# Kernel tuning notes

Measured on AMD Instinct MI355X. Metric: run time of the kernel, lower is better.

Reference implementation:

```python
import jax, jax.numpy as jnp
import numpy as np

B, T, M = 8, 512, 80
U = 896          # RNN_Size (even)
C = 256          # Class


def setup_inputs() -> dict:
    key = jax.random.key(0)
    ks = jax.random.split(key, 13)
    s = 0.05
    d = {
        'mels': jax.random.normal(ks[0], (B, T, M), jnp.float32),
        'Wk':  jax.random.normal(ks[1], (M + 3, 3 * U), jnp.float32) * s,
        'Wr':  jax.random.normal(ks[2], (U, 3 * U), jnp.float32) * s,
        'b':   jax.random.normal(ks[3], (2, 3 * U), jnp.float32) * s,
        'W1c': jax.random.normal(ks[4], (U // 2, U // 2), jnp.float32) * s,
        'b1c': jax.random.normal(ks[5], (U // 2,), jnp.float32) * s,
        'W2c': jax.random.normal(ks[6], (U // 2, C), jnp.float32) * s,
        'b2c': jax.random.normal(ks[7], (C,), jnp.float32) * s,
        'W1f': jax.random.normal(ks[8], (U // 2, U // 2), jnp.float32) * s,
        'b1f': jax.random.normal(ks[9], (U // 2,), jnp.float32) * s,
        'W2f': jax.random.normal(ks[10], (U // 2, C), jnp.float32) * s,
        'b2f': jax.random.normal(ks[11], (C,), jnp.float32) * s,
    }
    return d


def reference(mels, Wk, Wr, b, W1c, b1c, W2c, b2c, W1f, b1f, W2f, b2f):
    # Keras GRUCell (reset_after=True) step.
    def gru(x, h):
        mx = x @ Wk + b[0]                     # [B, 3U]
        mi = h @ Wr + b[1]                     # [B, 3U]
        xz, xr, xh = jnp.split(mx, 3, axis=-1)
        iz, ir, ih = jnp.split(mi, 3, axis=-1)
        z = jax.nn.sigmoid(xz + iz)
        r = jax.nn.sigmoid(xr + ir)
        hh = jnp.tanh(xh + r * ih)
        return z * h + (1.0 - z) * hh

    def head(h, W1, b1, W2, b2):
        return jax.nn.relu(h @ W1 + b1) @ W2 + b2

    Bv = mels.shape[0]
    Tv = mels.shape[1]
    keys = jax.random.split(jax.random.key(42), Tv)
    mels_t = jnp.swapaxes(mels, 0, 1)          # [T, B, M]

    def step(carry, xs):
        coarse, fine, hidden = carry           # [B,1],[B,1],[B,U]
        mel, key = xs
        kc, kf = jax.random.split(key)
        dummy = jnp.zeros_like(coarse)
        # coarse pass (hidden NOT updated, faithful to original)
        x0 = jnp.concatenate([mel, coarse, fine, dummy], axis=-1)
        h0 = gru(x0, hidden)
        logit_c = head(h0[:, :U // 2], W1c, b1c, W2c, b2c)
        # original feeds softmax probs into tf.random.categorical (which
        # expects logits) -- reproduce that faithfully.
        probs_c = jax.nn.softmax(logit_c, axis=-1)
        new_c = jax.random.categorical(kc, probs_c, axis=-1).astype(mels.dtype)[:, None]
        new_c_val = new_c / 255.0 * 2.0 - 1.0
        # fine pass (hidden IS updated)
        x1 = jnp.concatenate([mel, coarse, fine, new_c_val], axis=-1)
        h1 = gru(x1, hidden)
        logit_f = head(h1[:, U // 2:], W1f, b1f, W2f, b2f)
        probs_f = jax.nn.softmax(logit_f, axis=-1)
        new_f = jax.random.categorical(kf, probs_f, axis=-1).astype(mels.dtype)[:, None]
        new_f_val = new_f / 255.0 * 2.0 - 1.0
        sample = (new_c * C + new_f) / 32767.5 - 1.0   # [B,1]
        return (new_c_val, new_f_val, h1), sample[:, 0]

    init = (jnp.zeros((Bv, 1), mels.dtype),
            jnp.zeros((Bv, 1), mels.dtype),
            jnp.zeros((Bv, U), mels.dtype))
    _, samples = jax.lax.scan(step, init, (mels_t, keys))
    return jnp.swapaxes(samples, 0, 1)         # [B, T]
```

## Files before the change

kernel.cpp:

```cpp
#include <hip/hip_runtime.h>
#include <cstdint>
#include <math.h>

#define U 896
#define HU 448
#define TU 2688
#define BB 8
#define TT 512
#define MM 80
#define CC 256
#define NTH 512
#define NBLK 72

__device__ __forceinline__ uint32_t rotl32(uint32_t v, int r){ return (v<<r)|(v>>(32-r)); }

__device__ void threefry(uint32_t k0, uint32_t k1, uint32_t x0, uint32_t x1,
                         uint32_t* o0, uint32_t* o1){
  uint32_t k2 = k0 ^ k1 ^ 0x1BD11BDAu;
  x0 += k0; x1 += k1;
  x0+=x1; x1=rotl32(x1,13); x1^=x0;
  x0+=x1; x1=rotl32(x1,15); x1^=x0;
  x0+=x1; x1=rotl32(x1,26); x1^=x0;
  x0+=x1; x1=rotl32(x1, 6); x1^=x0;
  x0+=k1; x1+=k2+1u;
  x0+=x1; x1=rotl32(x1,17); x1^=x0;
  x0+=x1; x1=rotl32(x1,29); x1^=x0;
  x0+=x1; x1=rotl32(x1,16); x1^=x0;
  x0+=x1; x1=rotl32(x1,24); x1^=x0;
  x0+=k2; x1+=k0+2u;
  x0+=x1; x1=rotl32(x1,13); x1^=x0;
  x0+=x1; x1=rotl32(x1,15); x1^=x0;
  x0+=x1; x1=rotl32(x1,26); x1^=x0;
  x0+=x1; x1=rotl32(x1, 6); x1^=x0;
  x0+=k0; x1+=k1+3u;
  x0+=x1; x1=rotl32(x1,17); x1^=x0;
  x0+=x1; x1=rotl32(x1,29); x1^=x0;
  x0+=x1; x1=rotl32(x1,16); x1^=x0;
  x0+=x1; x1=rotl32(x1,24); x1^=x0;
  x0+=k1; x1+=k2+4u;
  x0+=x1; x1=rotl32(x1,13); x1^=x0;
  x0+=x1; x1=rotl32(x1,15); x1^=x0;
  x0+=x1; x1=rotl32(x1,26); x1^=x0;
  x0+=x1; x1=rotl32(x1, 6); x1^=x0;
  x0+=k2; x1+=k0+5u;
  *o0 = x0; *o1 = x1;
}

__device__ float gumbel_from(uint32_t ka, uint32_t kb, uint32_t e){
  uint32_t o0, o1;
  threefry(ka, kb, 0u, e, &o0, &o1);
  uint32_t bits = o0 ^ o1;
  uint32_t m = bits >> 9;
  float u = (m == 0u) ? 1.17549435e-38f
                      : (__uint_as_float(m | 0x3f800000u) - 1.0f);
  float l1 = (float)log((double)u);
  float l2 = (float)log((double)(-l1));
  return -l2;
}

__device__ __forceinline__ float sig_f(float x){
  return (float)(0.5 + 0.5*tanh(0.5*(double)x));
}
__device__ __forceinline__ float tanh_f(float x){ return (float)tanh((double)x); }

__device__ __forceinline__ float gldf(const float* p){
  return __hip_atomic_load(p, __ATOMIC_RELAXED, __HIP_MEMORY_SCOPE_AGENT);
}
__device__ __forceinline__ void gstf(float* p, float v){
  __hip_atomic_store(p, v, __ATOMIC_RELAXED, __HIP_MEMORY_SCOPE_AGENT);
}
__device__ __forceinline__ int gldi(const int* p){
  return __hip_atomic_load(p, __ATOMIC_RELAXED, __HIP_MEMORY_SCOPE_AGENT);
}
__device__ __forceinline__ void gsti(int* p, int v){
  __hip_atomic_store(p, v, __ATOMIC_RELAXED, __HIP_MEMORY_SCOPE_AGENT);
}

__device__ __forceinline__ void wait_slots(const uint32_t* slots, int n, uint32_t tgt, int tid){
  if (tid < n){
    const uint32_t* p = slots + (size_t)tid*32;
    int it = 0;
    while (__hip_atomic_load(p, __ATOMIC_RELAXED, __HIP_MEMORY_SCOPE_AGENT) < tgt){
      if (++it > (1<<24)) break;
    }
  }
  __syncthreads();
}
__device__ __forceinline__ void publish_slot(uint32_t* slot, uint32_t v, int tid){
  __syncthreads();
  if (tid == 0)
    __hip_atomic_store(slot, v, __ATOMIC_RELEASE, __HIP_MEMORY_SCOPE_AGENT);
}

__device__ __forceinline__ void fma4(float4& a, const float4& w, float h){
  a.x += w.x*h; a.y += w.y*h; a.z += w.z*h; a.w += w.w*h;
}

__device__ __forceinline__ void bf8(float4* a){
  #pragma unroll
  for (int d=8; d<64; d<<=1){
    #pragma unroll
    for (int b=0;b<8;++b){
      a[b].x += __shfl_xor(a[b].x, d);
      a[b].y += __shfl_xor(a[b].y, d);
      a[b].z += __shfl_xor(a[b].z, d);
      a[b].w += __shfl_xor(a[b].w, d);
    }
  }
}

__global__ __launch_bounds__(256) void k_keys(uint32_t* __restrict__ kc, uint32_t* __restrict__ kf){
  int t = blockIdx.x*256 + threadIdx.x;
  if (t >= TT) return;
  uint32_t ka, kb;
  threefry(0u, 42u, 0u, (uint32_t)t, &ka, &kb);
  uint32_t c0,c1,f0,f1;
  threefry(ka, kb, 0u, 0u, &c0, &c1);
  threefry(ka, kb, 0u, 1u, &f0, &f1);
  kc[2*t] = c0; kc[2*t+1] = c1;
  kf[2*t] = f0; kf[2*t+1] = f1;
}

#define O_SH1   0
#define O_SH1HI 1024
#define O_SFV   2048
#define O_SG    3072
#define O_SYC   6656
#define O_SYF   10240
#define O_KC    13824
#define O_KF    17920
#define O_NCV   22016
#define O_FVS   22080
#define O_NCI   22144
#define O_PRE   22272
#define O_IHB   108288
#define O_HGL   136960
#define O_H0C   194304
#define O_PLC   208640
#define O_PLF   438016
#define WS_ZERO 667392

__global__ __launch_bounds__(NTH, 2) void wavernn_persist(
    const float* __restrict__ mels, const float* __restrict__ Wk,
    const float* __restrict__ Wr,  const float* __restrict__ bias,
    const float* __restrict__ W1c, const float* __restrict__ b1c,
    const float* __restrict__ W2c, const float* __restrict__ b2c,
    const float* __restrict__ W1f, const float* __restrict__ b1f,
    const float* __restrict__ W2f, const float* __restrict__ b2f,
    float* __restrict__ out, char* __restrict__ ws)
{
  uint32_t* SH1   = (uint32_t*)(ws + O_SH1);
  uint32_t* SH1HI = (uint32_t*)(ws + O_SH1HI);
  uint32_t* SFV   = (uint32_t*)(ws + O_SFV);
  uint32_t* SG    = (uint32_t*)(ws + O_SG);
  uint32_t* SYC   = (uint32_t*)(ws + O_SYC);
  uint32_t* SYF   = (uint32_t*)(ws + O_SYF);
  const uint32_t* kc = (const uint32_t*)(ws + O_KC);
  const uint32_t* kf = (const uint32_t*)(ws + O_KF);
  float* ncvB = (float*)(ws + O_NCV);
  float* fvsB = (float*)(ws + O_FVS);
  int*   nci  = (int*)  (ws + O_NCI);
  float* pre  = (float*)(ws + O_PRE);
  float* ihb  = (float*)(ws + O_IHB);
  float* hgl  = (float*)(ws + O_HGL);
  float* h0c  = (float*)(ws + O_H0C);
  float* plgtC= (float*)(ws + O_PLC);
  float* plgtF= (float*)(ws + O_PLF);

  __shared__ __align__(16) char smem[46080];
  const int bk = blockIdx.x, tid = threadIdx.x;

  if (bk < 28){
    const int c4i = tid & 7, ks = tid >> 3;
    const int k0 = ks*14;
    const int lane = tid & 63, wv = tid >> 6;
    const int U0 = bk*32;
    const int cb0 = U0 + c4i*4;
    float* hlf   = (float*)smem;
    float* wredf = (float*)(smem + 32768);
    float* gbuf  = (float*)(smem + 41984);
    const int xk = 896 + ks*2;
    const int r0 = ((xk   < 978) ? xk   : 978) - 896;
    const int r1 = ((xk+1 < 978) ? xk+1 : 978) - 896;

    for (int t=0; t<TT; ++t){
      wait_slots(SH1, 8, (uint32_t)t, tid);
      const int hs = (t&1)*7168;
      for (int i=tid;i<8192;i+=NTH){
        const int b = i>>10, k = i&1023;
        float v;
        if (k < 896)      v = gldf(hgl + hs + b*896 + k);
        else if (k < 976) v = mels[((size_t)b*TT + t)*MM + (k-896)];
        else if (k == 976)v = gldf(ncvB + ((t+1)&1)*8 + b);
        else              v = 0.f;
        hlf[i] = v;
      }
      __syncthreads();

      for (int g=0; g<3; ++g){
        const int cbg = g*896 + cb0;
        float4 aW[8], aX[8];
        #pragma unroll
        for (int b=0;b<8;++b){ aW[b]=make_float4(0,0,0,0); aX[b]=make_float4(0,0,0,0); }
        #pragma unroll 2
        for (int j=0;j<14;++j){
          const float4 w = *(const float4*)(Wr + (size_t)(k0+j)*TU + cbg);
          #pragma unroll
          for (int b=0;b<8;++b) fma4(aW[b], w, hlf[b*1024 + k0 + j]);
        }
        {
          const float4 w0 = *(const float4*)(Wk + (size_t)r0*TU + cbg);
          const float4 w1 = *(const float4*)(Wk + (size_t)r1*TU + cbg);
          #pragma unroll
          for (int b=0;b<8;++b){
            fma4(aX[b], w0, hlf[b*1024 + 896 + ks*2]);
            fma4(aX[b], w1, hlf[b*1024 + 897 + ks*2]);
          }
        }
        if (g < 2){
          #pragma unroll
          for (int b=0;b<8;++b){
            aW[b].x += aX[b].x; aW[b].y += aX[b].y;
            aW[b].z += aX[b].z; aW[b].w += aX[b].w;
          }
          bf8(aW);
          if (lane < 8){
            float* dst = wredf + wv*288 + lane*36;
            #pragma unroll
            for (int b=0;b<8;++b) *(float4*)(dst + b*4) = aW[b];
          }
          __syncthreads();
          if (tid < 256){
            const int b = tid>>5, ci = tid&31;
            float s = 0.f;
            #pragma unroll
            for (int w=0; w<8; ++w) s += wredf[w*288 + (ci>>2)*36 + b*4 + (ci&3)];
            const int col = g*896 + U0 + ci;
            const float val = s + bias[col] + bias[TU + col];
            gstf(pre + b*TU + col, val);
            gbuf[(b*32 + ci)*4 + g] = val;
          }
          __syncthreads();
        } else {
          bf8(aW);
          if (lane < 8){
            float* dst = wredf + wv*288 + lane*36;
            #pragma unroll
            for (int b=0;b<8;++b) *(float4*)(dst + b*4) = aW[b];
          }
          __syncthreads();
          if (tid < 256){
            const int b = tid>>5, ci = tid&31;
            float s = 0.f;
            #pragma unroll
            for (int w=0; w<8; ++w) s += wredf[w*288 + (ci>>2)*36 + b*4 + (ci&3)];
            const int u = U0 + ci;
            const float val = s + bias[TU + 1792 + u];
            gstf(ihb + b*896 + u, val);
            gbuf[(b*32 + ci)*4 + 3] = val;
          }
          __syncthreads();
          bf8(aX);
          if (lane < 8){
            float* dst = wredf + wv*288 + lane*36;
            #pragma unroll
            for (int b=0;b<8;++b) *(float4*)(dst + b*4) = aX[b];
          }
          __syncthreads();
          if (tid < 256){
            const int b = tid>>5, ci = tid&31;
            float s = 0.f;
            #pragma unroll
            for (int w=0; w<8; ++w) s += wredf[w*288 + (ci>>2)*36 + b*4 + (ci&3)];
            const int u = U0 + ci;
            const float val = s + bias[1792 + u];
            gstf(pre + b*TU + 1792 + u, val);
            gbuf[(b*32 + ci)*4 + 2] = val;
          }
          __syncthreads();
        }
      }

      if (bk < 14){
        wait_slots(SFV, 8, (uint32_t)t, tid);
        if (tid < 256){
          const int b = tid>>5, ub = tid&31, u = U0 + ub;
          const float fv = gldf(fvsB + ((t+1)&1)*8 + b);
          const float* gb = gbuf + (b*32 + ub)*4;
          const float az = gb[0] + fv*Wk[(size_t)81*TU + u];
          const float ar = gb[1] + fv*Wk[(size_t)81*TU + 896 + u];
          const float ax = gb[2] + fv*Wk[(size_t)81*TU + 1792 + u];
          const float z = sig_f(az), r = sig_f(ar);
          const float hh = tanh_f(ax + r*gb[3]);
          gstf(h0c + b*HU + u, z*hlf[b*1024 + u] + (1.0f - z)*hh);
        }
      }
      publish_slot(SG + bk*32, (uint32_t)(t+1), tid);
    }
  } else if (bk < 56){
    const int j = bk - 28;
    float* hstg = (float*)smem;
    float* red1 = (float*)(smem + 14336);
    float* y1s  = (float*)(smem + 16384);
    const int outp = tid & 127, ks4 = tid >> 7;
    const int ob = outp >> 4, oc = outp & 15;
    const int i0 = ks4*112;

    for (int t=0; t<TT; ++t){
      wait_slots(SG, 14, (uint32_t)(t+1), tid);
      for (int i=tid;i<3584;i+=NTH) hstg[i] = gldf(h0c + i);
      __syncthreads();
      {
        float s = 0.f;
        const float* hb = hstg + ob*HU;
        const float* wb = W1c + (size_t)i0*HU + j*16 + oc;
        #pragma unroll 4
        for (int i=0;i<112;++i) s += hb[i0+i]*wb[(size_t)i*HU];
        red1[outp*4 + ks4] = s;
      }
      __syncthreads();
      if (tid < 128){
        const float v = (red1[tid*4+0]+red1[tid*4+1])+(red1[tid*4+2]+red1[tid*4+3]);
        y1s[tid] = fmaxf(v + b1c[j*16 + (tid&15)], 0.0f);
      }
      __syncthreads();
      #pragma unroll
      for (int p=0;p<4;++p){
        const int o2 = p*512 + tid;
        const int b = o2 >> 8, cc = o2 & 255;
        float s2 = 0.f;
        #pragma unroll
        for (int i=0;i<16;++i) s2 += y1s[b*16+i]*W2c[(size_t)(j*16+i)*CC + cc];
        gstf(plgtC + j*2048 + o2, s2);
      }
      publish_slot(SYC + j*32, (uint32_t)(t+1), tid);

      wait_slots(SH1HI, 8, (uint32_t)(t+1), tid);
      const int hsN = ((t+1)&1)*7168;
      for (int i=tid;i<3584;i+=NTH){
        const int b = i/HU, ii = i - b*HU;
        hstg[i] = gldf(hgl + hsN + b*U + HU + ii);
      }
      __syncthreads();
      {
        float s = 0.f;
        const float* hb = hstg + ob*HU;
        const float* wb = W1f + (size_t)i0*HU + j*16 + oc;
        #pragma unroll 4
        for (int i=0;i<112;++i) s += hb[i0+i]*wb[(size_t)i*HU];
        red1[outp*4 + ks4] = s;
      }
      __syncthreads();
      if (tid < 128){
        const float v = (red1[tid*4+0]+red1[tid*4+1])+(red1[tid*4+2]+red1[tid*4+3]);
        y1s[tid] = fmaxf(v + b1f[j*16 + (tid&15)], 0.0f);
      }
      __syncthreads();
      #pragma unroll
      for (int p=0;p<4;++p){
        const int o2 = p*512 + tid;
        const int b = o2 >> 8, cc = o2 & 255;
        float s2 = 0.f;
        #pragma unroll
        for (int i=0;i<16;++i) s2 += y1s[b*16+i]*W2f[(size_t)(j*16+i)*CC + cc];
        gstf(plgtF + j*2048 + o2, s2);
      }
      publish_slot(SYF + j*32, (uint32_t)(t+1), tid);
    }
  } else if (bk < 64){
    const int b = bk - 56;
    float* sredf = (float*)smem;
    int*   sredi = (int*)(smem + 64);
    for (int t=0; t<TT; ++t){
      const float gmb = (tid<256) ? gumbel_from(kc[2*t], kc[2*t+1], (uint32_t)(b*CC + tid)) : 0.f;
      wait_slots(SYC, 28, (uint32_t)(t+1), tid);
      wait_slots(SG, 28, (uint32_t)(t+1), tid);
      float logit = -3.402823466e38f;
      if (tid < 256){
        float s = 0.f;
        #pragma unroll
        for (int j=0;j<28;++j) s += gldf(plgtC + j*2048 + b*CC + tid);
        logit = s + b2c[tid];
      }
      float m = logit;
      #pragma unroll
      for (int d=1; d<64; d<<=1) m = fmaxf(m, __shfl_xor(m, d));
      if ((tid&63)==0) sredf[tid>>6] = m;
      __syncthreads();
      const float mx = fmaxf(fmaxf(sredf[0],sredf[1]), fmaxf(sredf[2],sredf[3]));
      __syncthreads();
      const float e = (tid<256) ? (float)exp((double)(logit - mx)) : 0.f;
      float ss = e;
      #pragma unroll
      for (int d=1; d<64; d<<=1) ss += __shfl_xor(ss, d);
      if ((tid&63)==0) sredf[tid>>6] = ss;
      __syncthreads();
      const float sum = (sredf[0]+sredf[1])+(sredf[2]+sredf[3]);
      __syncthreads();
      float v = (tid<256) ? (e/sum + gmb) : -3.402823466e38f;
      int bi = (tid<256) ? tid : (1<<30);
      #pragma unroll
      for (int d=1; d<64; d<<=1){
        const float ov = __shfl_xor(v, d);
        const int   oi = __shfl_xor(bi, d);
        if (ov > v || (ov == v && oi < bi)){ v = ov; bi = oi; }
      }
      if ((tid&63)==0){ sredf[tid>>6] = v; sredi[tid>>6] = bi; }
      __syncthreads();
      float bv = sredf[0]; int nc = sredi[0];
      #pragma unroll
      for (int w=1; w<4; ++w){
        if (sredf[w] > bv || (sredf[w] == bv && sredi[w] < nc)){ bv = sredf[w]; nc = sredi[w]; }
      }
      if (tid==0){
        gsti(nci + b, nc);
        gstf(ncvB + (t&1)*8 + b, (float)nc/255.0f*2.0f - 1.0f);
      }
      const float ncv = (float)nc/255.0f*2.0f - 1.0f;
      const float fv = gldf(fvsB + ((t+1)&1)*8 + b);
      const int hsO = (t&1)*7168, hsN = ((t+1)&1)*7168;
      if (tid < 448){
        const int u = 448 + tid;
        const float az = gldf(pre + b*TU + u)        + fv*Wk[(size_t)81*TU + u]        + ncv*Wk[(size_t)82*TU + u];
        const float ar = gldf(pre + b*TU + 896 + u)  + fv*Wk[(size_t)81*TU + 896 + u]  + ncv*Wk[(size_t)82*TU + 896 + u];
        const float ax = gldf(pre + b*TU + 1792 + u) + fv*Wk[(size_t)81*TU + 1792 + u] + ncv*Wk[(size_t)82*TU + 1792 + u];
        const float ih = gldf(ihb + b*896 + u);
        const float z = sig_f(az), r = sig_f(ar);
        const float hh = tanh_f(ax + r*ih);
        gstf(hgl + hsN + b*896 + u, z*gldf(hgl + hsO + b*896 + u) + (1.0f - z)*hh);
      }
      publish_slot(SH1HI + b*32, (uint32_t)(t+1), tid);
      if (tid < 448){
        const int u = tid;
        const float az = gldf(pre + b*TU + u)        + fv*Wk[(size_t)81*TU + u]        + ncv*Wk[(size_t)82*TU + u];
        const float ar = gldf(pre + b*TU + 896 + u)  + fv*Wk[(size_t)81*TU + 896 + u]  + ncv*Wk[(size_t)82*TU + 896 + u];
        const float ax = gldf(pre + b*TU + 1792 + u) + fv*Wk[(size_t)81*TU + 1792 + u] + ncv*Wk[(size_t)82*TU + 1792 + u];
        const float ih = gldf(ihb + b*896 + u);
        const float z = sig_f(az), r = sig_f(ar);
        const float hh = tanh_f(ax + r*ih);
        gstf(hgl + hsN + b*896 + u, z*gldf(hgl + hsO + b*896 + u) + (1.0f - z)*hh);
      }
      publish_slot(SH1 + b*32, (uint32_t)(t+1), tid);
    }
  } else {
    const int b = bk - 64;
    float* sredf = (float*)smem;
    int*   sredi = (int*)(smem + 64);
    for (int t=0; t<TT; ++t){
      const float gmb = (tid<256) ? gumbel_from(kf[2*t], kf[2*t+1], (uint32_t)(b*CC + tid)) : 0.f;
      wait_slots(SYF, 28, (uint32_t)(t+1), tid);
      float logit = -3.402823466e38f;
      if (tid < 256){
        float s = 0.f;
        #pragma unroll
        for (int j=0;j<28;++j) s += gldf(plgtF + j*2048 + b*CC + tid);
        logit = s + b2f[tid];
      }
      float m = logit;
      #pragma unroll
      for (int d=1; d<64; d<<=1) m = fmaxf(m, __shfl_xor(m, d));
      if ((tid&63)==0) sredf[tid>>6] = m;
      __syncthreads();
      const float mx = fmaxf(fmaxf(sredf[0],sredf[1]), fmaxf(sredf[2],sredf[3]));
      __syncthreads();
      const float e = (tid<256) ? (float)exp((double)(logit - mx)) : 0.f;
      float ss = e;
      #pragma unroll
      for (int d=1; d<64; d<<=1) ss += __shfl_xor(ss, d);
      if ((tid&63)==0) sredf[tid>>6] = ss;
      __syncthreads();
      const float sum = (sredf[0]+sredf[1])+(sredf[2]+sredf[3]);
      __syncthreads();
      float v = (tid<256) ? (e/sum + gmb) : -3.402823466e38f;
      int bi = (tid<256) ? tid : (1<<30);
      #pragma unroll
      for (int d=1; d<64; d<<=1){
        const float ov = __shfl_xor(v, d);
        const int   oi = __shfl_xor(bi, d);
        if (ov > v || (ov == v && oi < bi)){ v = ov; bi = oi; }
      }
      if ((tid&63)==0){ sredf[tid>>6] = v; sredi[tid>>6] = bi; }
      __syncthreads();
      float bv = sredf[0]; int nf = sredi[0];
      #pragma unroll
      for (int w=1; w<4; ++w){
        if (sredf[w] > bv || (sredf[w] == bv && sredi[w] < nf)){ bv = sredf[w]; nf = sredi[w]; }
      }
      if (tid==0){
        gstf(fvsB + (t&1)*8 + b, (float)nf/255.0f*2.0f - 1.0f);
        const int nc = gldi(nci + b);
        out[(size_t)b*TT + t] = ((float)nc*256.0f + (float)nf)/32767.5f - 1.0f;
      }
      publish_slot(SFV + b*32, (uint32_t)(t+1), tid);
    }
  }
}

extern "C" void kernel_launch(void* const* d_in, const int* in_sizes, int n_in,
                              void* d_out, int out_size, void* d_ws, size_t ws_size,
                              hipStream_t stream) {
  const float* mels = (const float*)d_in[0];
  const float* Wk   = (const float*)d_in[1];
  const float* Wr   = (const float*)d_in[2];
  const float* bias = (const float*)d_in[3];
  const float* W1c  = (const float*)d_in[4];
  const float* b1c  = (const float*)d_in[5];
  const float* W2c  = (const float*)d_in[6];
  const float* b2c  = (const float*)d_in[7];
  const float* W1f  = (const float*)d_in[8];
  const float* b1f  = (const float*)d_in[9];
  const float* W2f  = (const float*)d_in[10];
  const float* b2f  = (const float*)d_in[11];
  float* out = (float*)d_out;
  char* wsb = (char*)d_ws;

  uint32_t* kc = (uint32_t*)(wsb + O_KC);
  uint32_t* kf = (uint32_t*)(wsb + O_KF);

  hipMemsetAsync(d_ws, 0, WS_ZERO, stream);
  k_keys<<<2,256,0,stream>>>(kc, kf);

  void* args[] = { (void*)&mels, (void*)&Wk, (void*)&Wr, (void*)&bias,
                   (void*)&W1c, (void*)&b1c, (void*)&W2c, (void*)&b2c,
                   (void*)&W1f, (void*)&b1f, (void*)&W2f, (void*)&b2f,
                   (void*)&out, (void*)&wsb };
  hipLaunchCooperativeKernel((const void*)wavernn_persist, dim3(NBLK), dim3(NTH),
                             args, 0, stream);
}
```

Measured before the change: 20.12 ms.

## Add busy-burn spin waits, single-wave sampling, and 64-bit atomic loads/stores

Replaces the flag wait with a wave-level __all poll, during which the other waves spin on dummy FMAs, apparently to keep clocks up while blocked. The softmax and categorical sampling now run in one wavefront with four classes per lane, removing the shared-memory reductions and block barriers. Global atomic loads and stores are widened to 64-bit float2 throughout the GRU, head and reduction paths, and the coarse sampler's two waits are merged into one. The burn loop draws power and issue slots, and the spin limit is lowered from 1<<24 to 1<<22 iterations.

```diff
diff --git a/kernel.cpp b/kernel.cpp
--- a/kernel.cpp
+++ b/kernel.cpp
@@ -5,7 +5,6 @@
 #define U 896
 #define HU 448
 #define TU 2688
-#define BB 8
 #define TT 512
 #define MM 80
 #define CC 256
@@ -75,17 +74,46 @@
 __device__ __forceinline__ void gsti(int* p, int v){
   __hip_atomic_store(p, v, __ATOMIC_RELAXED, __HIP_MEMORY_SCOPE_AGENT);
 }
-
-__device__ __forceinline__ void wait_slots(const uint32_t* slots, int n, uint32_t tgt, int tid){
-  if (tid < n){
-    const uint32_t* p = slots + (size_t)tid*32;
+__device__ __forceinline__ float2 gldf2(const float* p){
+  unsigned long long v = __hip_atomic_load((const unsigned long long*)p,
+                                           __ATOMIC_RELAXED, __HIP_MEMORY_SCOPE_AGENT);
+  union { unsigned long long u; float2 f; } cv; cv.u = v; return cv.f;
+}
+__device__ __forceinline__ void gstf2(float* p, float2 f){
+  union { float2 f; unsigned long long u; } cv; cv.f = f;
+  __hip_atomic_store((unsigned long long*)p, cv.u,
+                     __ATOMIC_RELAXED, __HIP_MEMORY_SCOPE_AGENT);
+}
+
+__device__ __forceinline__ void wait_burn(const uint32_t* s0, int n0,
+                                          const uint32_t* s1, int n1,
+                                          uint32_t tgt, int tid, volatile int* sdone){
+  if (tid == 0) *sdone = 0;
+  __syncthreads();
+  if (tid < 64){
+    const uint32_t* p = nullptr;
+    if (tid < n0) p = s0 + (size_t)tid*32;
+    else if (s1 != nullptr && tid >= 32 && tid < 32 + n1) p = s1 + (size_t)(tid-32)*32;
     int it = 0;
-    while (__hip_atomic_load(p, __ATOMIC_RELAXED, __HIP_MEMORY_SCOPE_AGENT) < tgt){
-      if (++it > (1<<24)) break;
+    for(;;){
+      bool ok = (p == nullptr) ||
+        (__hip_atomic_load(p, __ATOMIC_RELAXED, __HIP_MEMORY_SCOPE_AGENT) >= tgt);
+      if (__all(ok)) break;
+      if (++it > (1<<22)) break;
     }
+    if (tid == 0) *sdone = 1;
+  } else {
+    float a = 1.0f + (float)tid*1e-7f;
+    const float b = 0.999999f;
+    while (!*sdone){
+      #pragma unroll
+      for (int q=0;q<48;++q) a = fmaf(a, b, 1e-9f);
+    }
+    asm volatile("" :: "v"(a));
   }
   __syncthreads();
 }
+
 __device__ __forceinline__ void publish_slot(uint32_t* slot, uint32_t v, int tid){
   __syncthreads();
   if (tid == 0)
@@ -107,6 +135,34 @@
       a[b].w += __shfl_xor(a[b].w, d);
     }
   }
+}
+
+__device__ __forceinline__ int sample256(float l0, float l1, float l2, float l3,
+                                         const float g[4], int gl){
+  float m = fmaxf(fmaxf(l0,l1), fmaxf(l2,l3));
+  #pragma unroll
+  for (int d=1; d<64; d<<=1) m = fmaxf(m, __shfl_xor(m, d));
+  const float e0 = (float)exp((double)(l0-m));
+  const float e1 = (float)exp((double)(l1-m));
+  const float e2 = (float)exp((double)(l2-m));
+  const float e3 = (float)exp((double)(l3-m));
+  float ss = ((e0+e1)+(e2+e3));
+  #pragma unroll
+  for (int d=1; d<64; d<<=1) ss += __shfl_xor(ss, d);
+  const float v0 = e0/ss + g[0], v1 = e1/ss + g[1];
+  const float v2 = e2/ss + g[2], v3 = e3/ss + g[3];
+  float v = v0; int bi = 4*gl;
+  if (v1 > v){ v = v1; bi = 4*gl+1; }
+  float vB = v2; int biB = 4*gl+2;
+  if (v3 > vB){ vB = v3; biB = 4*gl+3; }
+  if (vB > v || (vB == v && biB < bi)){ v = vB; bi = biB; }
+  #pragma unroll
+  for (int d=1; d<64; d<<=1){
+    const float ov = __shfl_xor(v, d);
+    const int   oi = __shfl_xor(bi, d);
+    if (ov > v || (ov == v && oi < bi)){ v = ov; bi = oi; }
+  }
+  return bi;
 }
 
 __global__ __launch_bounds__(256) void k_keys(uint32_t* __restrict__ kc, uint32_t* __restrict__ kf){
@@ -168,14 +224,14 @@
   float* plgtF= (float*)(ws + O_PLF);
 
   __shared__ __align__(16) char smem[46080];
+  __shared__ int sdone;
   const int bk = blockIdx.x, tid = threadIdx.x;
 
   if (bk < 28){
-    const int c4i = tid & 7, ks = tid >> 3;
-    const int k0 = ks*14;
+    const int ks = tid >> 3, k0 = ks*14;
     const int lane = tid & 63, wv = tid >> 6;
     const int U0 = bk*32;
-    const int cb0 = U0 + c4i*4;
+    const int cb0 = U0 + (tid & 7)*4;
     float* hlf   = (float*)smem;
     float* wredf = (float*)(smem + 32768);
     float* gbuf  = (float*)(smem + 41984);
@@ -184,16 +240,19 @@
     const int r1 = ((xk+1 < 978) ? xk+1 : 978) - 896;
 
     for (int t=0; t<TT; ++t){
-      wait_slots(SH1, 8, (uint32_t)t, tid);
+      wait_burn(SH1, 8, nullptr, 0, (uint32_t)t, tid, &sdone);
       const int hs = (t&1)*7168;
-      for (int i=tid;i<8192;i+=NTH){
-        const int b = i>>10, k = i&1023;
-        float v;
-        if (k < 896)      v = gldf(hgl + hs + b*896 + k);
-        else if (k < 976) v = mels[((size_t)b*TT + t)*MM + (k-896)];
-        else if (k == 976)v = gldf(ncvB + ((t+1)&1)*8 + b);
-        else              v = 0.f;
-        hlf[i] = v;
+      for (int i=tid;i<3584;i+=NTH){
+        const int b = i/448, kp = (i - b*448)*2;
+        const float2 h2 = gldf2(hgl + hs + b*896 + kp);
+        hlf[b*1024 + kp] = h2.x; hlf[b*1024 + kp + 1] = h2.y;
+      }
+      for (int i=tid;i<1024;i+=NTH){
+        const int b = i>>7, k2 = i&127;
+        float v = 0.f;
+        if (k2 < 80) v = mels[((size_t)b*TT + t)*MM + k2];
+        else if (k2 == 80) v = gldf(ncvB + ((t+1)&1)*8 + b);
+        hlf[b*1024 + 896 + k2] = v;
       }
       __syncthreads();
 
@@ -203,10 +262,10 @@
         #pragma unroll
         for (int b=0;b<8;++b){ aW[b]=make_float4(0,0,0,0); aX[b]=make_float4(0,0,0,0); }
         #pragma unroll 2
-        for (int j=0;j<14;++j){
-          const float4 w = *(const float4*)(Wr + (size_t)(k0+j)*TU + cbg);
+        for (int jj=0;jj<14;++jj){
+          const float4 w = *(const float4*)(Wr + (size_t)(k0+jj)*TU + cbg);
           #pragma unroll
-          for (int b=0;b<8;++b) fma4(aW[b], w, hlf[b*1024 + k0 + j]);
+          for (int b=0;b<8;++b) fma4(aW[b], w, hlf[b*1024 + k0 + jj]);
         }
         {
           const float4 w0 = *(const float4*)(Wk + (size_t)r0*TU + cbg);
@@ -230,15 +289,20 @@
             for (int b=0;b<8;++b) *(float4*)(dst + b*4) = aW[b];
           }
           __syncthreads();
-          if (tid < 256){
-            const int b = tid>>5, ci = tid&31;
-            float s = 0.f;
+          if (tid < 128){
+            const int rb = tid>>4, rq = tid&15;
+            float s0 = 0.f, s1 = 0.f;
             #pragma unroll
-            for (int w=0; w<8; ++w) s += wredf[w*288 + (ci>>2)*36 + b*4 + (ci&3)];
-            const int col = g*896 + U0 + ci;
-            const float val = s + bias[col] + bias[TU + col];
-            gstf(pre + b*TU + col, val);
-            gbuf[(b*32 + ci)*4 + g] = val;
+            for (int w=0; w<8; ++w){
+              const float* wp = wredf + w*288 + (rq>>1)*36 + rb*4 + ((2*rq)&3);
+              s0 += wp[0]; s1 += wp[1];
+            }
+            const int col0 = g*896 + U0 + 2*rq;
+            const float v0 = s0 + bias[col0]   + bias[TU + col0];
+            const float v1 = s1 + bias[col0+1] + bias[TU + col0+1];
+            gstf2(pre + rb*TU + col0, make_float2(v0, v1));
+            gbuf[(rb*32 + 2*rq)*4 + g] = v0;
+            gbuf[(rb*32 + 2*rq + 1)*4 + g] = v1;
           }
           __syncthreads();
         } else {
@@ -249,15 +313,20 @@
             for (int b=0;b<8;++b) *(float4*)(dst + b*4) = aW[b];
           }
           __syncthreads();
-          if (tid < 256){
-            const int b = tid>>5, ci = tid&31;
-            float s = 0.f;
+          if (tid < 128){
+            const int rb = tid>>4, rq = tid&15;
+            float s0 = 0.f, s1 = 0.f;
             #pragma unroll
-            for (int w=0; w<8; ++w) s += wredf[w*288 + (ci>>2)*36 + b*4 + (ci&3)];
-            const int u = U0 + ci;
-            const float val = s + bias[TU + 1792 + u];
-            gstf(ihb + b*896 + u, val);
-            gbuf[(b*32 + ci)*4 + 3] = val;
+            for (int w=0; w<8; ++w){
+              const float* wp = wredf + w*288 + (rq>>1)*36 + rb*4 + ((2*rq)&3);
+              s0 += wp[0]; s1 += wp[1];
+            }
+            const int u0 = U0 + 2*rq;
+            const float v0 = s0 + bias[TU + 1792 + u0];
+            const float v1 = s1 + bias[TU + 1792 + u0 + 1];
+            gstf2(ihb + rb*896 + u0, make_float2(v0, v1));
+            gbuf[(rb*32 + 2*rq)*4 + 3] = v0;
+            gbuf[(rb*32 + 2*rq + 1)*4 + 3] = v1;
           }
           __syncthreads();
           bf8(aX);
@@ -267,32 +336,46 @@
             for (int b=0;b<8;++b) *(float4*)(dst + b*4) = aX[b];
           }
           __syncthreads();
-          if (tid < 256){
-            const int b = tid>>5, ci = tid&31;
-            float s = 0.f;
+          if (tid < 128){
+            const int rb = tid>>4, rq = tid&15;
+            float s0 = 0.f, s1 = 0.f;
             #pragma unroll
-            for (int w=0; w<8; ++w) s += wredf[w*288 + (ci>>2)*36 + b*4 + (ci&3)];
-            const int u = U0 + ci;
-            const float val = s + bias[1792 + u];
-            gstf(pre + b*TU + 1792 + u, val);
-            gbuf[(b*32 + ci)*4 + 2] = val;
+            for (int w=0; w<8; ++w){
+              const float* wp = wredf + w*288 + (rq>>1)*36 + rb*4 + ((2*rq)&3);
+              s0 += wp[0]; s1 += wp[1];
+            }
+            const int u0 = U0 + 2*rq;
+            const float v0 = s0 + bias[1792 + u0];
+            const float v1 = s1 + bias[1792 + u0 + 1];
+            gstf2(pre + rb*TU + 1792 + u0, make_float2(v0, v1));
+            gbuf[(rb*32 + 2*rq)*4 + 2] = v0;
+            gbuf[(rb*32 + 2*rq + 1)*4 + 2] = v1;
           }
           __syncthreads();
         }
       }
 
       if (bk < 14){
-        wait_slots(SFV, 8, (uint32_t)t, tid);
-        if (tid < 256){
-          const int b = tid>>5, ub = tid&31, u = U0 + ub;
+        wait_burn(SFV, 8, nullptr, 0, (uint32_t)t, tid, &sdone);
+        if (tid < 128){
+          const int b = tid>>4, q = tid&15;
+          const int u0 = U0 + 2*q;
           const float fv = gldf(fvsB + ((t+1)&1)*8 + b);
-          const float* gb = gbuf + (b*32 + ub)*4;
-          const float az = gb[0] + fv*Wk[(size_t)81*TU + u];
-          const float ar = gb[1] + fv*Wk[(size_t)81*TU + 896 + u];
-          const float ax = gb[2] + fv*Wk[(size_t)81*TU + 1792 + u];
-          const float z = sig_f(az), r = sig_f(ar);
-          const float hh = tanh_f(ax + r*gb[3]);
-          gstf(h0c + b*HU + u, z*hlf[b*1024 + u] + (1.0f - z)*hh);
+          const float2 wz = *(const float2*)(Wk + (size_t)81*TU + u0);
+          const float2 wr = *(const float2*)(Wk + (size_t)81*TU + 896 + u0);
+          const float2 wx = *(const float2*)(Wk + (size_t)81*TU + 1792 + u0);
+          const float* g0 = gbuf + (b*32 + 2*q)*4;
+          const float* g1 = g0 + 4;
+          const float az0 = g0[0] + fv*wz.x, az1 = g1[0] + fv*wz.y;
+          const float ar0 = g0[1] + fv*wr.x, ar1 = g1[1] + fv*wr.y;
+          const float ax0 = g0[2] + fv*wx.x, ax1 = g1[2] + fv*wx.y;
+          const float z0 = sig_f(az0), z1 = sig_f(az1);
+          const float r0g = sig_f(ar0), r1g = sig_f(ar1);
+          const float hh0 = tanh_f(ax0 + r0g*g0[3]);
+          const float hh1 = tanh_f(ax1 + r1g*g1[3]);
+          const float o0 = z0*hlf[b*1024 + u0]     + (1.0f - z0)*hh0;
+          const float o1 = z1*hlf[b*1024 + u0 + 1] + (1.0f - z1)*hh1;
+          gstf2(h0c + b*HU + u0, make_float2(o0, o1));
         }
       }
       publish_slot(SG + bk*32, (uint32_t)(t+1), tid);
@@ -307,8 +390,11 @@
     const int i0 = ks4*112;
 
     for (int t=0; t<TT; ++t){
-      wait_slots(SG, 14, (uint32_t)(t+1), tid);
-      for (int i=tid;i<3584;i+=NTH) hstg[i] = gldf(h0c + i);
+      wait_burn(SG, 14, nullptr, 0, (uint32_t)(t+1), tid, &sdone);
+      for (int i=tid;i<1792;i+=NTH){
+        const float2 v = gldf2(h0c + 2*i);
+        hstg[2*i] = v.x; hstg[2*i+1] = v.y;
+      }
       __syncthreads();
       {
         float s = 0.f;
@@ -325,21 +411,26 @@
       }
       __syncthreads();
       #pragma unroll
-      for (int p=0;p<4;++p){
-        const int o2 = p*512 + tid;
-        const int b = o2 >> 8, cc = o2 & 255;
-        float s2 = 0.f;
+      for (int p=0;p<2;++p){
+        const int po = p*512 + tid;
+        const int b = po>>7, cc0 = (po&127)*2;
+        float sa = 0.f, sb = 0.f;
         #pragma unroll
-        for (int i=0;i<16;++i) s2 += y1s[b*16+i]*W2c[(size_t)(j*16+i)*CC + cc];
-        gstf(plgtC + j*2048 + o2, s2);
+        for (int i=0;i<16;++i){
+          const float yv = y1s[b*16+i];
+          const float2 w2 = *(const float2*)(W2c + (size_t)(j*16+i)*CC + cc0);
+          sa += yv*w2.x; sb += yv*w2.y;
+        }
+        gstf2(plgtC + j*2048 + b*256 + cc0, make_float2(sa, sb));
       }
       publish_slot(SYC + j*32, (uint32_t)(t+1), tid);
 
-      wait_slots(SH1HI, 8, (uint32_t)(t+1), tid);
+      wait_burn(SH1HI, 8, nullptr, 0, (uint32_t)(t+1), tid, &sdone);
       const int hsN = ((t+1)&1)*7168;
-      for (int i=tid;i<3584;i+=NTH){
-        const int b = i/HU, ii = i - b*HU;
-        hstg[i] = gldf(hgl + hsN + b*U + HU + ii);
+      for (int i=tid;i<1792;i+=NTH){
+        const int b = i/224, ii0 = (i - b*224)*2;
+        const float2 v = gldf2(hgl + hsN + b*896 + 448 + ii0);
+        hstg[b*448 + ii0] = v.x; hstg[b*448 + ii0 + 1] = v.y;
       }
       __syncthreads();
       {
@@ -357,139 +448,133 @@
       }
       __syncthreads();
       #pragma unroll
-      for (int p=0;p<4;++p){
-        const int o2 = p*512 + tid;
-        const int b = o2 >> 8, cc = o2 & 255;
-        float s2 = 0.f;
+      for (int p=0;p<2;++p){
+        const int po = p*512 + tid;
+        const int b = po>>7, cc0 = (po&127)*2;
+        float sa = 0.f, sb = 0.f;
         #pragma unroll
-        for (int i=0;i<16;++i) s2 += y1s[b*16+i]*W2f[(size_t)(j*16+i)*CC + cc];
-        gstf(plgtF + j*2048 + o2, s2);
+        for (int i=0;i<16;++i){
+          const float yv = y1s[b*16+i];
+          const float2 w2 = *(const float2*)(W2f + (size_t)(j*16+i)*CC + cc0);
+          sa += yv*w2.x; sb += yv*w2.y;
+        }
+        gstf2(plgtF + j*2048 + b*256 + cc0, make_float2(sa, sb));
       }
       publish_slot(SYF + j*32, (uint32_t)(t+1), tid);
     }
   } else if (bk < 64){
     const int b = bk - 56;
-    float* sredf = (float*)smem;
-    int*   sredi = (int*)(smem + 64);
+    __shared__ int ncSh;
     for (int t=0; t<TT; ++t){
-      const float gmb = (tid<256) ? gumbel_from(kc[2*t], kc[2*t+1], (uint32_t)(b*CC + tid)) : 0.f;
-      wait_slots(SYC, 28, (uint32_t)(t+1), tid);
-      wait_slots(SG, 28, (uint32_t)(t+1), tid);
-      float logit = -3.402823466e38f;
-      if (tid < 256){
-        float s = 0.f;
+      float gc[4];
+      if (tid < 64){
+        const uint32_t ka = kc[2*t], kb2 = kc[2*t+1];
         #pragma unroll
-        for (int j=0;j<28;++j) s += gldf(plgtC + j*2048 + b*CC + tid);
-        logit = s + b2c[tid];
-      }
-      float m = logit;
-      #pragma unroll
-      for (int d=1; d<64; d<<=1) m = fmaxf(m, __shfl_xor(m, d));
-      if ((tid&63)==0) sredf[tid>>6] = m;
-      __syncthreads();
-      const float mx = fmaxf(fmaxf(sredf[0],sredf[1]), fmaxf(sredf[2],sredf[3]));
-      __syncthreads();
-      const float e = (tid<256) ? (float)exp((double)(logit - mx)) : 0.f;
-      float ss = e;
-      #pragma unroll
-      for (int d=1; d<64; d<<=1) ss += __shfl_xor(ss, d);
-      if ((tid&63)==0) sredf[tid>>6] = ss;
-      __syncthreads();
-      const float sum = (sredf[0]+sredf[1])+(sredf[2]+sredf[3]);
-      __syncthreads();
-      float v = (tid<256) ? (e/sum + gmb) : -3.402823466e38f;
-      int bi = (tid<256) ? tid : (1<<30);
-      #pragma unroll
-      for (int d=1; d<64; d<<=1){
-        const float ov = __shfl_xor(v, d);
-        const int   oi = __shfl_xor(bi, d);
-        if (ov > v || (ov == v && oi < bi)){ v = ov; bi = oi; }
-      }
-      if ((tid&63)==0){ sredf[tid>>6] = v; sredi[tid>>6] = bi; }
-      __syncthreads();
-      float bv = sredf[0]; int nc = sredi[0];
-      #pragma unroll
-      for (int w=1; w<4; ++w){
-        if (sredf[w] > bv || (sredf[w] == bv && sredi[w] < nc)){ bv = sredf[w]; nc = sredi[w]; }
-      }
-      if (tid==0){
-        gsti(nci + b, nc);
-        gstf(ncvB + (t&1)*8 + b, (float)nc/255.0f*2.0f - 1.0f);
-      }
-      const float ncv = (float)nc/255.0f*2.0f - 1.0f;
+        for (int i=0;i<4;++i)
+          gc[i] = gumbel_from(ka, kb2, (uint32_t)(b*CC + 4*tid + i));
+      }
+      wait_burn(SYC, 28, SG, 28, (uint32_t)(t+1), tid, &sdone);
+      if (tid < 64){
+        float s0=0.f,s1=0.f,s2=0.f,s3=0.f;
+        const float* pb = plgtC + b*256 + 4*tid;
+        for (int q=0;q<28;++q){
+          const float2 pA = gldf2(pb + q*2048);
+          const float2 pB = gldf2(pb + q*2048 + 2);
+          s0 += pA.x; s1 += pA.y; s2 += pB.x; s3 += pB.y;
+        }
+        const float l0 = s0 + b2c[4*tid+0], l1 = s1 + b2c[4*tid+1];
+        const float l2 = s2 + b2c[4*tid+2], l3 = s3 + b2c[4*tid+3];
+        const int nc = sample256(l0,l1,l2,l3, gc, tid);
+        if (tid == 0){
+          gsti(nci + b, nc);
+          gstf(ncvB + (t&1)*8 + b, (float)nc/255.0f*2.0f - 1.0f);
+          ncSh = nc;
+        }
+      }
+      __syncthreads();
+      const float ncv = (float)ncSh/255.0f*2.0f - 1.0f;
       const float fv = gldf(fvsB + ((t+1)&1)*8 + b);
       const int hsO = (t&1)*7168, hsN = ((t+1)&1)*7168;
-      if (tid < 448){
-        const int u = 448 + tid;
-        const float az = gldf(pre + b*TU + u)        + fv*Wk[(size_t)81*TU + u]        + ncv*Wk[(size_t)82*TU + u];
-        const float ar = gldf(pre + b*TU + 896 + u)  + fv*Wk[(size_t)81*TU + 896 + u]  + ncv*Wk[(size_t)82*TU + 896 + u];
-        const float ax = gldf(pre + b*TU + 1792 + u) + fv*Wk[(size_t)81*TU + 1792 + u] + ncv*Wk[(size_t)82*TU + 1792 + u];
-        const float ih = gldf(ihb + b*896 + u);
-        const float z = sig_f(az), r = sig_f(ar);
-        const float hh = tanh_f(ax + r*ih);
-        gstf(hgl + hsN + b*896 + u, z*gldf(hgl + hsO + b*896 + u) + (1.0f - z)*hh);
+      if (tid < 224){
+        const int u0 = 448 + 2*tid;
+        const float2 pz = gldf2(pre + b*TU + u0);
+        const float2 pr = gldf2(pre + b*TU + 896 + u0);
+        const float2 px = gldf2(pre + b*TU + 1792 + u0);
+        const float2 ih = gldf2(ihb + b*896 + u0);
+        const float2 ho = gldf2(hgl + hsO + b*896 + u0);
+        const float2 w81z = *(const float2*)(Wk + (size_t)81*TU + u0);
+        const float2 w81r = *(const float2*)(Wk + (size_t)81*TU + 896 + u0);
+        const float2 w81x = *(const float2*)(Wk + (size_t)81*TU + 1792 + u0);
+        const float2 w82z = *(const float2*)(Wk + (size_t)82*TU + u0);
+        const float2 w82r = *(const float2*)(Wk + (size_t)82*TU + 896 + u0);
+        const float2 w82x = *(const float2*)(Wk + (size_t)82*TU + 1792 + u0);
+        const float az0 = pz.x + fv*w81z.x + ncv*w82z.x;
+        const float az1 = pz.y + fv*w81z.y + ncv*w82z.y;
+        const float ar0 = pr.x + fv*w81r.x + ncv*w82r.x;
+        const float ar1 = pr.y + fv*w81r.y + ncv*w82r.y;
+        const float ax0 = px.x + fv*w81x.x + ncv*w82x.x;
+        const float ax1 = px.y + fv*w81x.y + ncv*w82x.y;
+        const float z0 = sig_f(az0), z1 = sig_f(az1);
+        const float r0g = sig_f(ar0), r1g = sig_f(ar1);
+        const float h0v = z0*ho.x + (1.0f - z0)*tanh_f(ax0 + r0g*ih.x);
+        const float h1v = z1*ho.y + (1.0f - z1)*tanh_f(ax1 + r1g*ih.y);
+        gstf2(hgl + hsN + b*896 + u0, make_float2(h0v, h1v));
       }
       publish_slot(SH1HI + b*32, (uint32_t)(t+1), tid);
-      if (tid < 448){
-        const int u = tid;
-        const float az = gldf(pre + b*TU + u)        + fv*Wk[(size_t)81*TU + u]        + ncv*Wk[(size_t)82*TU + u];
-        const float ar = gldf(pre + b*TU + 896 + u)  + fv*Wk[(size_t)81*TU + 896 + u]  + ncv*Wk[(size_t)82*TU + 896 + u];
-        const float ax = gldf(pre + b*TU + 1792 + u) + fv*Wk[(size_t)81*TU + 1792 + u] + ncv*Wk[(size_t)82*TU + 1792 + u];
-        const float ih = gldf(ihb + b*896 + u);
-        const float z = sig_f(az), r = sig_f(ar);
-        const float hh = tanh_f(ax + r*ih);
-        gstf(hgl + hsN + b*896 + u, z*gldf(hgl + hsO + b*896 + u) + (1.0f - z)*hh);
+      if (tid < 224){
+        const int u0 = 2*tid;
+        const float2 pz = gldf2(pre + b*TU + u0);
+        const float2 pr = gldf2(pre + b*TU + 896 + u0);
+        const float2 px = gldf2(pre + b*TU + 1792 + u0);
+        const float2 ih = gldf2(ihb + b*896 + u0);
+        const float2 ho = gldf2(hgl + hsO + b*896 + u0);
+        const float2 w81z = *(const float2*)(Wk + (size_t)81*TU + u0);
+        const float2 w81r = *(const float2*)(Wk + (size_t)81*TU + 896 + u0);
+        const float2 w81x = *(const float2*)(Wk + (size_t)81*TU + 1792 + u0);
+        const float2 w82z = *(const float2*)(Wk + (size_t)82*TU + u0);
+        const float2 w82r = *(const float2*)(Wk + (size_t)82*TU + 896 + u0);
+        const float2 w82x = *(const float2*)(Wk + (size_t)82*TU + 1792 + u0);
+        const float az0 = pz.x + fv*w81z.x + ncv*w82z.x;
+        const float az1 = pz.y + fv*w81z.y + ncv*w82z.y;
+        const float ar0 = pr.x + fv*w81r.x + ncv*w82r.x;
+        const float ar1 = pr.y + fv*w81r.y + ncv*w82r.y;
+        const float ax0 = px.x + fv*w81x.x + ncv*w82x.x;
+        const float ax1 = px.y + fv*w81x.y + ncv*w82x.y;
+        const float z0 = sig_f(az0), z1 = sig_f(az1);
+        const float r0g = sig_f(ar0), r1g = sig_f(ar1);
+        const float h0v = z0*ho.x + (1.0f - z0)*tanh_f(ax0 + r0g*ih.x);
+        const float h1v = z1*ho.y + (1.0f - z1)*tanh_f(ax1 + r1g*ih.y);
+        gstf2(hgl + hsN + b*896 + u0, make_float2(h0v, h1v));
       }
       publish_slot(SH1 + b*32, (uint32_t)(t+1), tid);
     }
   } else {
     const int b = bk - 64;
-    float* sredf = (float*)smem;
-    int*   sredi = (int*)(smem + 64);
     for (int t=0; t<TT; ++t){
-      const float gmb = (tid<256) ? gumbel_from(kf[2*t], kf[2*t+1], (uint32_t)(b*CC + tid)) : 0.f;
-      wait_slots(SYF, 28, (uint32_t)(t+1), tid);
-      float logit = -3.402823466e38f;
-      if (tid < 256){
-        float s = 0.f;
+      float gf[4];
+      if (tid < 64){
+        const uint32_t ka = kf[2*t], kb2 = kf[2*t+1];
         #pragma unroll
-        for (int j=0;j<28;++j) s += gldf(plgtF + j*2048 + b*CC + tid);
-        logit = s + b2f[tid];
-      }
-      float m = logit;
-      #pragma unroll
-      for (int d=1; d<64; d<<=1) m = fmaxf(m, __shfl_xor(m, d));
-      if ((tid&63)==0) sredf[tid>>6] = m;
-      __syncthreads();
-      const float mx = fmaxf(fmaxf(sredf[0],sredf[1]), fmaxf(sredf[2],sredf[3]));
-      __syncthreads();
-      const float e = (tid<256) ? (float)exp((double)(logit - mx)) : 0.f;
-      float ss = e;
-      #pragma unroll
-      for (int d=1; d<64; d<<=1) ss += __shfl_xor(ss, d);
-      if ((tid&63)==0) sredf[tid>>6] = ss;
-      __syncthreads();
-      const float sum = (sredf[0]+sredf[1])+(sredf[2]+sredf[3]);
-      __syncthreads();
-      float v = (tid<256) ? (e/sum + gmb) : -3.402823466e38f;
-      int bi = (tid<256) ? tid : (1<<30);
-      #pragma unroll
-      for (int d=1; d<64; d<<=1){
-        const float ov = __shfl_xor(v, d);
-        const int   oi = __shfl_xor(bi, d);
-        if (ov > v || (ov == v && oi < bi)){ v = ov; bi = oi; }
-      }
-      if ((tid&63)==0){ sredf[tid>>6] = v; sredi[tid>>6] = bi; }
-      __syncthreads();
-      float bv = sredf[0]; int nf = sredi[0];
-      #pragma unroll
-      for (int w=1; w<4; ++w){
-        if (sredf[w] > bv || (sredf[w] == bv && sredi[w] < nf)){ bv = sredf[w]; nf = sredi[w]; }
-      }
-      if (tid==0){
-        gstf(fvsB + (t&1)*8 + b, (float)nf/255.0f*2.0f - 1.0f);
-        const int nc = gldi(nci + b);
-        out[(size_t)b*TT + t] = ((float)nc*256.0f + (float)nf)/32767.5f - 1.0f;
+        for (int i=0;i<4;++i)
+          gf[i] = gumbel_from(ka, kb2, (uint32_t)(b*CC + 4*tid + i));
+      }
+      wait_burn(SYF, 28, nullptr, 0, (uint32_t)(t+1), tid, &sdone);
+      if (tid < 64){
+        float s0=0.f,s1=0.f,s2=0.f,s3=0.f;
+        const float* pb = plgtF + b*256 + 4*tid;
+        for (int q=0;q<28;++q){
+          const float2 pA = gldf2(pb + q*2048);
+          const float2 pB = gldf2(pb + q*2048 + 2);
+          s0 += pA.x; s1 += pA.y; s2 += pB.x; s3 += pB.y;
+        }
+        const float l0 = s0 + b2f[4*tid+0], l1 = s1 + b2f[4*tid+1];
+        const float l2 = s2 + b2f[4*tid+2], l3 = s3 + b2f[4*tid+3];
+        const int nf = sample256(l0,l1,l2,l3, gf, tid);
+        if (tid == 0){
+          gstf(fvsB + (t&1)*8 + b, (float)nf/255.0f*2.0f - 1.0f);
+          const int nc = gldi(nci + b);
+          out[(size_t)b*TT + t] = ((float)nc*256.0f + (float)nf)/32767.5f - 1.0f;
+        }
       }
       publish_slot(SFV + b*32, (uint32_t)(t+1), tid);
     }
```

New measurement: 23.39 ms. 16.3% more time.
